# Performance work log

Hardware: AMD Instinct MI355X
Metric: run time of the kernel (lower is better)

## Reference

```python
import jax, jax.numpy as jnp
import numpy as np

_DN = ('NDHWC', 'DHWIO', 'NDHWC')

def _deconv(x, w, b, stride):
    # kernel-3 transposed conv; SAME padding -> out spatial = in * stride
    y = jax.lax.conv_transpose(x, w, strides=(stride, stride, stride),
                               padding='SAME', dimension_numbers=_DN)
    return y + b


def setup_inputs() -> dict:
    key = jax.random.key(0)
    ks = jax.random.split(key, 14)
    C = 128

    def w(k, cin, cout):
        std = 1.0 / np.sqrt(27.0 * cin)  # fan-in init, kernel 3^3
        return jax.random.normal(k, (3, 3, 3, cin, cout), jnp.float32) * std

    def b(k, cout):
        return jax.random.normal(k, (cout,), jnp.float32) * 0.01

    return {
        'x':   jax.random.normal(ks[0], (1, 8, 8, 8, C), jnp.float32),
        'w0':  w(ks[1], C, C),  'b0':  b(ks[2], C),
        'w00': w(ks[3], C, C),  'b00': b(ks[4], C),
        'w1':  w(ks[5], C, C),  'b1':  b(ks[6], C),
        'w10': w(ks[7], C, C),  'b10': b(ks[8], C),
        'w2':  w(ks[9], C, 64), 'b2':  b(ks[10], 64),
        'w20': w(ks[11], 64, 3), 'b20': b(ks[12], 3),
    }


def reference(x, w0, b0, w00, b00, w1, b1, w10, b10, w2, b2, w20, b20):
    # deconv0 (stride 2) -> deconv0_0 (stride 1) -> ReLU
    out = jax.nn.relu(_deconv(_deconv(x, w0, b0, 2), w00, b00, 1))
    # deconv1 (stride 2) -> deconv1_0 (stride 1) -> ReLU
    out = jax.nn.relu(_deconv(_deconv(out, w1, b1, 2), w10, b10, 1))
    # deconv2 (stride 2, C->64) -> deconv2_0 (stride 1, 64->3)
    out = _deconv(_deconv(out, w2, b2, 2), w20, b20, 1)
    return out
```

## Files before the change

kernel.cpp:

```cpp
#include <hip/hip_runtime.h>


typedef __attribute__((ext_vector_type(8))) short bf16x8;
typedef __attribute__((ext_vector_type(8))) _Float16 f16x8;
typedef __attribute__((ext_vector_type(4))) float f32x4;
typedef unsigned short u16;

__device__ __forceinline__ u16 f2bf(float f) {
    unsigned u = __builtin_bit_cast(unsigned, f);
    u += 0x7fffu + ((u >> 16) & 1u);
    return (u16)(u >> 16);
}
__device__ __forceinline__ float bf2f(u16 h) {
    unsigned u = ((unsigned)h) << 16;
    return __builtin_bit_cast(float, u);
}
__device__ __forceinline__ void split_store(float v, u16* ph, u16* pl) {
    u16 h = f2bf(v);
    *ph = h;
    *pl = f2bf(v - bf2f(h));
}
__device__ __forceinline__ u16 f2h(float v) {
    return __builtin_bit_cast(u16, (_Float16)v);
}
__device__ __forceinline__ int swz(int bx, int G) { return (bx & 7) * (G >> 3) + (bx >> 3); }

__global__ __launch_bounds__(256) void pack_all(
    const float* __restrict__ x, float* __restrict__ zf,
    u16* __restrict__ Xh, u16* __restrict__ Xl,
    const float* __restrict__ w0_, const float* __restrict__ w1_,
    const float* __restrict__ w2_, const float* __restrict__ w3_,
    const float* __restrict__ w4_, const float* __restrict__ w5_,
    u16* s0h, u16* s0l, u16* s1h, u16* s1l, u16* s2h, u16* s2l,
    u16* s3h, u16* s3l, u16* s4h, u16* s4l, u16* s5h, u16* s5l)
{
    if (blockIdx.y == 6) {
        if (blockIdx.x < 64) {
            const int i = (blockIdx.x * 256 + threadIdx.x) * 4;
            const float4 v = *(const float4*)(x + i);
            split_store(v.x, Xh + i,     Xl + i);
            split_store(v.y, Xh + i + 1, Xl + i + 1);
            split_store(v.z, Xh + i + 2, Xl + i + 2);
            split_store(v.w, Xh + i + 3, Xl + i + 3);
        } else if (blockIdx.x == 64) {
            ((float4*)zf)[threadIdx.x] = make_float4(0.f, 0.f, 0.f, 0.f);
        }
        return;
    }
    const float* w; u16 *bh, *bl; int Cin, Cout, nNt;
    switch (blockIdx.y) {
        case 0: w = w0_; bh = s0h; bl = s0l; Cin = 128; Cout = 128; nNt = 8; break;
        case 1: w = w1_; bh = s1h; bl = s1l; Cin = 128; Cout = 128; nNt = 8; break;
        case 2: w = w2_; bh = s2h; bl = s2l; Cin = 128; Cout = 128; nNt = 8; break;
        case 3: w = w3_; bh = s3h; bl = s3l; Cin = 128; Cout = 128; nNt = 8; break;
        case 4: w = w4_; bh = s4h; bl = s4l; Cin = 128; Cout = 64;  nNt = 4; break;
        default:w = w5_; bh = s5h; bl = s5l; Cin = 64;  Cout = 3;   nNt = 1; break;
    }
    const bool f16 = (blockIdx.y >= 1);
    const int KC = Cin >> 5;
    const int total = 27 * nNt * KC * 64;
    int t = blockIdx.x * 256 + threadIdx.x;
    if (t >= total) return;
    const int lane = t & 63;
    int r = t >> 6;
    const int kc = r % KC; r /= KC;
    const int nt = r % nNt; r /= nNt;
    const int tap = r;
    const int n  = nt * 16 + (lane & 15);
    const int k0 = kc * 32 + (lane >> 4) * 8;
    const size_t o = (size_t)t * 8;
    for (int j = 0; j < 8; ++j) {
        float v = (n < Cout) ? w[((size_t)tap * Cin + k0 + j) * Cout + n] : 0.f;
        if (f16) {
            const _Float16 h = (_Float16)v;
            bh[o + j] = __builtin_bit_cast(u16, h);
            bl[o + j] = f2h(v - (float)h);
        } else {
            const u16 h = f2bf(v);
            bh[o + j] = h;
            bl[o + j] = f2bf(v - bf2f(h));
        }
    }
}

template<int CIN, int MT, int NT>
__global__ __launch_bounds__(64) void deconv_s2_bf16(
    const u16* __restrict__ Ah, const u16* __restrict__ Al,
    const u16* __restrict__ Bh, const u16* __restrict__ Bl,
    const float* __restrict__ bias, const u16* __restrict__ Z,
    u16* __restrict__ Y, int Din, int lD, int Cout, int nNtTot)
{
    constexpr int KC = CIN >> 5;
    const int Dout = 2 * Din;
    const int lane = threadIdx.x;
    const int ml = lane & 15, kq = lane >> 4;
    const int M0 = swz(blockIdx.x, gridDim.x) * (MT * 16);
    const int N0t = blockIdx.y * NT;
    const int par = blockIdx.z;
    const int rd = (par >> 2) & 1, rh = (par >> 1) & 1, rw = par & 1;

    int sw[MT], sh[MT], sd[MT];
    #pragma unroll
    for (int mt = 0; mt < MT; ++mt) {
        const int sv = M0 + mt * 16 + ml;
        sw[mt] = sv & (Din - 1); sh[mt] = (sv >> lD) & (Din - 1); sd[mt] = sv >> (2 * lD);
    }

    f32x4 acc[MT][NT];
    #pragma unroll
    for (int nt = 0; nt < NT; ++nt) {
        const float bv = bias[(N0t + nt) * 16 + ml];
        #pragma unroll
        for (int mt = 0; mt < MT; ++mt) acc[mt][nt] = (f32x4){bv, bv, bv, bv};
    }

    const int lw = rw ? 0 : 1, lh = rh ? 0 : 1, ld2 = rd ? 0 : 1;
    const int ntap = 1 << (lw + lh + ld2);

    const u16 *pah[MT], *pal[MT];
    size_t fb;
    auto set_tap = [&](int t) {
        const int tw_ = t & ((1 << lw) - 1);
        const int th_ = (t >> lw) & ((1 << lh) - 1);
        const int td_ = t >> (lw + lh);
        const int kd = rd ? 1 : (td_ ? 0 : 2);
        const int kh = rh ? 1 : (th_ ? 0 : 2);
        const int kw = rw ? 1 : (tw_ ? 0 : 2);
        const int dd = rd ? 0 : -td_, dh = rh ? 0 : -th_, dw = rw ? 0 : -tw_;
        const int tap = (kd * 3 + kh) * 3 + kw;
        #pragma unroll
        for (int mt = 0; mt < MT; ++mt) {
            const int id = sd[mt] + dd, ih = sh[mt] + dh, iw = sw[mt] + dw;
            const bool v = id >= 0 && ih >= 0 && iw >= 0;
            const size_t off = (size_t)((id * Din + ih) * Din + iw) * CIN;
            pah[mt] = v ? Ah + off : Z;
            pal[mt] = v ? Al + off : Z;
        }
        fb = ((size_t)tap * nNtTot + N0t) * KC;
    };

    bf16x8 fah[2][MT], fal[2][MT], fbh[2][NT], fbl[2][NT];
    auto load_frags = [&](int buf, int kc) {
        const int ko = kc * 32 + kq * 8;
        #pragma unroll
        for (int mt = 0; mt < MT; ++mt) {
            fah[buf][mt] = *(const bf16x8*)(pah[mt] + ko);
            fal[buf][mt] = *(const bf16x8*)(pal[mt] + ko);
        }
        #pragma unroll
        for (int nt = 0; nt < NT; ++nt) {
            const size_t fo = (fb + (size_t)nt * KC + kc) * 512 + lane * 8;
            fbh[buf][nt] = *(const bf16x8*)(Bh + fo);
            fbl[buf][nt] = *(const bf16x8*)(Bl + fo);
        }
    };

    set_tap(0);
    load_frags(0, 0);

    for (int t = 0; t < ntap; ++t) {
        #pragma unroll
        for (int kc = 0; kc < KC; ++kc) {
            const int cur = kc & 1, nxt = cur ^ 1;
            if (kc + 1 < KC) {
                load_frags(nxt, kc + 1);
            } else {
                set_tap(t + 1 < ntap ? t + 1 : t);
                load_frags(nxt, 0);
            }
            #pragma unroll
            for (int mt = 0; mt < MT; ++mt)
            #pragma unroll
            for (int nt = 0; nt < NT; ++nt) {
                acc[mt][nt] = __builtin_amdgcn_mfma_f32_16x16x32_bf16(fah[cur][mt], fbh[cur][nt], acc[mt][nt], 0, 0, 0);
                acc[mt][nt] = __builtin_amdgcn_mfma_f32_16x16x32_bf16(fah[cur][mt], fbl[cur][nt], acc[mt][nt], 0, 0, 0);
                acc[mt][nt] = __builtin_amdgcn_mfma_f32_16x16x32_bf16(fal[cur][mt], fbh[cur][nt], acc[mt][nt], 0, 0, 0);
            }
        }
    }

    #pragma unroll
    for (int mt = 0; mt < MT; ++mt) {
        #pragma unroll
        for (int r = 0; r < 4; ++r) {
            const int sv = M0 + mt * 16 + kq * 4 + r;
            const int svw = sv & (Din - 1), svh = (sv >> lD) & (Din - 1), svd = sv >> (2 * lD);
            const int od = 2 * svd + rd, oh = 2 * svh + rh, ow = 2 * svw + rw;
            const size_t yb = (size_t)((od * Dout + oh) * Dout + ow) * Cout;
            #pragma unroll
            for (int nt = 0; nt < NT; ++nt)
                Y[yb + (N0t + nt) * 16 + ml] = f2h(acc[mt][nt][r]);
        }
    }
}

template<int CIN, int MT, int NT, bool RELU>
__global__ __launch_bounds__(64) void conv_s1_f16(
    const u16* __restrict__ A, const u16* __restrict__ Bh, const u16* __restrict__ Bl,
    const float* __restrict__ bias, const u16* __restrict__ Z,
    u16* __restrict__ Y, int D, int lD, int Cout, int nNtTot)
{
    constexpr int KC = CIN >> 5;
    const int lane = threadIdx.x;
    const int ml = lane & 15, kq = lane >> 4;
    const int M0 = swz(blockIdx.x, gridDim.x) * (MT * 16);
    const int N0t = blockIdx.y * NT;

    int vw[MT], vh[MT], vd[MT];
    #pragma unroll
    for (int mt = 0; mt < MT; ++mt) {
        const int vox = M0 + mt * 16 + ml;
        vw[mt] = vox & (D - 1); vh[mt] = (vox >> lD) & (D - 1); vd[mt] = vox >> (2 * lD);
    }

    f32x4 acc[MT][NT];
    #pragma unroll
    for (int nt = 0; nt < NT; ++nt) {
        const float bv = bias[(N0t + nt) * 16 + ml];
        #pragma unroll
        for (int mt = 0; mt < MT; ++mt) acc[mt][nt] = (f32x4){bv, bv, bv, bv};
    }

    const u16* pa[MT];
    size_t fb;
    auto set_tap = [&](int tap) {
        const int kd = tap / 9, kh = (tap % 9) / 3, kw = tap % 3;
        #pragma unroll
        for (int mt = 0; mt < MT; ++mt) {
            const int id = vd[mt] + kd - 1, ih = vh[mt] + kh - 1, iw = vw[mt] + kw - 1;
            const bool v = (unsigned)id < (unsigned)D && (unsigned)ih < (unsigned)D &&
                           (unsigned)iw < (unsigned)D;
            pa[mt] = v ? A + (size_t)((id * D + ih) * D + iw) * CIN : Z;
        }
        fb = ((size_t)tap * nNtTot + N0t) * KC;
    };

    f16x8 fa[2][MT], fbh[2][NT], fbl[2][NT];
    auto load_frags = [&](int buf, int kc) {
        const int ko = kc * 32 + kq * 8;
        #pragma unroll
        for (int mt = 0; mt < MT; ++mt)
            fa[buf][mt] = *(const f16x8*)(pa[mt] + ko);
        #pragma unroll
        for (int nt = 0; nt < NT; ++nt) {
            const size_t fo = (fb + (size_t)nt * KC + kc) * 512 + lane * 8;
            fbh[buf][nt] = *(const f16x8*)(Bh + fo);
            fbl[buf][nt] = *(const f16x8*)(Bl + fo);
        }
    };

    set_tap(0);
    load_frags(0, 0);

    for (int tap = 0; tap < 27; ++tap) {
        #pragma unroll
        for (int kc = 0; kc < KC; ++kc) {
            const int cur = kc & 1, nxt = cur ^ 1;
            if (kc + 1 < KC) {
                load_frags(nxt, kc + 1);
            } else {
                set_tap(tap < 26 ? tap + 1 : 26);
                load_frags(nxt, 0);
            }
            #pragma unroll
            for (int mt = 0; mt < MT; ++mt)
            #pragma unroll
            for (int nt = 0; nt < NT; ++nt) {
                acc[mt][nt] = __builtin_amdgcn_mfma_f32_16x16x32_f16(fa[cur][mt], fbh[cur][nt], acc[mt][nt], 0, 0, 0);
                acc[mt][nt] = __builtin_amdgcn_mfma_f32_16x16x32_f16(fa[cur][mt], fbl[cur][nt], acc[mt][nt], 0, 0, 0);
            }
        }
    }

    #pragma unroll
    for (int mt = 0; mt < MT; ++mt) {
        const int vox0 = M0 + mt * 16 + kq * 4;
        #pragma unroll
        for (int nt = 0; nt < NT; ++nt) {
            const int co = (N0t + nt) * 16 + ml;
            #pragma unroll
            for (int r = 0; r < 4; ++r) {
                float v = acc[mt][nt][r];
                if (RELU) v = fmaxf(v, 0.f);
                Y[(size_t)(vox0 + r) * Cout + co] = f2h(v);
            }
        }
    }
}

template<int CIN, int MT, int NT>
__global__ __launch_bounds__(64) void deconv_s2_f16(
    const u16* __restrict__ A, const u16* __restrict__ Bh, const u16* __restrict__ Bl,
    const float* __restrict__ bias, const u16* __restrict__ Z,
    u16* __restrict__ Y, int Din, int lD, int Cout, int nNtTot)
{
    constexpr int KC = CIN >> 5;
    const int Dout = 2 * Din;
    const int lane = threadIdx.x;
    const int ml = lane & 15, kq = lane >> 4;
    const int M0 = swz(blockIdx.x, gridDim.x) * (MT * 16);
    const int N0t = blockIdx.y * NT;
    const int par = blockIdx.z;
    const int rd = (par >> 2) & 1, rh = (par >> 1) & 1, rw = par & 1;

    int sw[MT], sh[MT], sd[MT];
    #pragma unroll
    for (int mt = 0; mt < MT; ++mt) {
        const int sv = M0 + mt * 16 + ml;
        sw[mt] = sv & (Din - 1); sh[mt] = (sv >> lD) & (Din - 1); sd[mt] = sv >> (2 * lD);
    }

    f32x4 acc[MT][NT];
    #pragma unroll
    for (int nt = 0; nt < NT; ++nt) {
        const float bv = bias[(N0t + nt) * 16 + ml];
        #pragma unroll
        for (int mt = 0; mt < MT; ++mt) acc[mt][nt] = (f32x4){bv, bv, bv, bv};
    }

    const int lw = rw ? 0 : 1, lh = rh ? 0 : 1, ld2 = rd ? 0 : 1;
    const int ntap = 1 << (lw + lh + ld2);

    const u16* pa[MT];
    size_t fb;
    auto set_tap = [&](int t) {
        const int tw_ = t & ((1 << lw) - 1);
        const int th_ = (t >> lw) & ((1 << lh) - 1);
        const int td_ = t >> (lw + lh);
        const int kd = rd ? 1 : (td_ ? 0 : 2);
        const int kh = rh ? 1 : (th_ ? 0 : 2);
        const int kw = rw ? 1 : (tw_ ? 0 : 2);
        const int dd = rd ? 0 : -td_, dh = rh ? 0 : -th_, dw = rw ? 0 : -tw_;
        const int tap = (kd * 3 + kh) * 3 + kw;
        #pragma unroll
        for (int mt = 0; mt < MT; ++mt) {
            const int id = sd[mt] + dd, ih = sh[mt] + dh, iw = sw[mt] + dw;
            const bool v = id >= 0 && ih >= 0 && iw >= 0;
            pa[mt] = v ? A + (size_t)((id * Din + ih) * Din + iw) * CIN : Z;
        }
        fb = ((size_t)tap * nNtTot + N0t) * KC;
    };

    f16x8 fa[2][MT], fbh[2][NT], fbl[2][NT];
    auto load_frags = [&](int buf, int kc) {
        const int ko = kc * 32 + kq * 8;
        #pragma unroll
        for (int mt = 0; mt < MT; ++mt)
            fa[buf][mt] = *(const f16x8*)(pa[mt] + ko);
        #pragma unroll
        for (int nt = 0; nt < NT; ++nt) {
            const size_t fo = (fb + (size_t)nt * KC + kc) * 512 + lane * 8;
            fbh[buf][nt] = *(const f16x8*)(Bh + fo);
            fbl[buf][nt] = *(const f16x8*)(Bl + fo);
        }
    };

    set_tap(0);
    load_frags(0, 0);

    for (int t = 0; t < ntap; ++t) {
        #pragma unroll
        for (int kc = 0; kc < KC; ++kc) {
            const int cur = kc & 1, nxt = cur ^ 1;
            if (kc + 1 < KC) {
                load_frags(nxt, kc + 1);
            } else {
                set_tap(t + 1 < ntap ? t + 1 : t);
                load_frags(nxt, 0);
            }
            #pragma unroll
            for (int mt = 0; mt < MT; ++mt)
            #pragma unroll
            for (int nt = 0; nt < NT; ++nt) {
                acc[mt][nt] = __builtin_amdgcn_mfma_f32_16x16x32_f16(fa[cur][mt], fbh[cur][nt], acc[mt][nt], 0, 0, 0);
                acc[mt][nt] = __builtin_amdgcn_mfma_f32_16x16x32_f16(fa[cur][mt], fbl[cur][nt], acc[mt][nt], 0, 0, 0);
            }
        }
    }

    #pragma unroll
    for (int mt = 0; mt < MT; ++mt) {
        #pragma unroll
        for (int r = 0; r < 4; ++r) {
            const int sv = M0 + mt * 16 + kq * 4 + r;
            const int svw = sv & (Din - 1), svh = (sv >> lD) & (Din - 1), svd = sv >> (2 * lD);
            const int od = 2 * svd + rd, oh = 2 * svh + rh, ow = 2 * svw + rw;
            const size_t yb = (size_t)((od * Dout + oh) * Dout + ow) * Cout;
            #pragma unroll
            for (int nt = 0; nt < NT; ++nt)
                Y[yb + (N0t + nt) * 16 + ml] = f2h(acc[mt][nt][r]);
        }
    }
}

template<int D, int R, bool RELU>
__global__ __launch_bounds__(256) void conv_s1_lds_f16(
    const u16* __restrict__ A, const u16* __restrict__ Bh, const u16* __restrict__ Bl,
    const float* __restrict__ bias, u16* __restrict__ Y)
{
    constexpr int SH  = R + 2;
    constexpr int SW  = D + 2;
    constexpr int VST = 72;
    __shared__ u16 sm[3 * SH * SW * VST];

    const int tid  = threadIdx.x;
    const int lane = tid & 63, widx = tid >> 6;
    const int ml = lane & 15, kq = lane >> 4;

    const int bpp = D / R;
    const int lb  = swz(blockIdx.x, gridDim.x);
    const int d   = lb / bpp;
    const int h0  = (lb % bpp) * R;
    const int N0  = widx * 2;

    f32x4 acc[4][2];
    #pragma unroll
    for (int nt = 0; nt < 2; ++nt) {
        const float bv = bias[(N0 + nt) * 16 + ml];
        #pragma unroll
        for (int mt = 0; mt < 4; ++mt) acc[mt][nt] = (f32x4){bv, bv, bv, bv};
    }

    for (int i = tid; i < 3 * SH * 2 * 8; i += 256) {
        const int slot = i >> 3, c8 = i & 7;
        const int side = slot & 1, rr = slot >> 1;
        const int dd = rr / SH, hh = rr % SH;
        *(f16x8*)(sm + ((dd * SH + hh) * SW + (side ? SW - 1 : 0)) * VST + c8 * 8) =
            (f16x8){0,0,0,0,0,0,0,0};
    }

    f16x8 cb[2][2][2], nb[2][2][2];
    auto loadB = [&](f16x8 (&dst)[2][2][2], int kcp, int tap) {
        #pragma unroll
        for (int nt = 0; nt < 2; ++nt)
        #pragma unroll
        for (int kcl = 0; kcl < 2; ++kcl) {
            const size_t fo = (((size_t)tap * 8 + N0 + nt) * 4 + kcp * 2 + kcl) * 512
                            + lane * 8;
            dst[nt][kcl][0] = *(const f16x8*)(Bh + fo);
            dst[nt][kcl][1] = *(const f16x8*)(Bl + fo);
        }
    };
    loadB(cb, 0, 0);

    for (int kcp = 0; kcp < 2; ++kcp) {
        __syncthreads();
        constexpr int NCH = 3 * SH * D * 8;
        for (int i = tid; i < NCH; i += 256) {
            const int vox = i >> 3, c8 = i & 7;
            const int ww = vox % D;
            const int rr = vox / D;
            const int hh = rr % SH, dd = rr / SH;
            const int pd = d + dd - 1, ph = h0 + hh - 1;
            u16* dst = sm + ((dd * SH + hh) * SW + ww + 1) * VST + c8 * 8;
            if ((unsigned)pd < (unsigned)D && (unsigned)ph < (unsigned)D) {
                const size_t g = ((size_t)(pd * D + ph) * D + ww) * 128 + kcp * 64 + c8 * 8;
                *(f16x8*)dst = *(const f16x8*)(A + g);
            } else {
                *(f16x8*)dst = (f16x8){0,0,0,0,0,0,0,0};
            }
        }
        __syncthreads();

        for (int tap = 0; tap < 27; ++tap) {
            const int lin = kcp * 27 + tap + 1;
            if (lin < 54) loadB(nb, lin / 27, lin % 27);
            const int kd = tap / 9, kh = (tap % 9) / 3, kw = tap % 3;
            f16x8 fa[4][2];
            #pragma unroll
            for (int mt = 0; mt < 4; ++mt) {
                const int m = mt * 16 + ml;
                const int mh = m / D, mw = m % D;
                const u16* p = sm + (((kd * SH) + (mh + kh)) * SW + (mw + kw)) * VST;
                fa[mt][0] = *(const f16x8*)(p + kq * 8);
                fa[mt][1] = *(const f16x8*)(p + 32 + kq * 8);
            }
            #pragma unroll
            for (int mt = 0; mt < 4; ++mt)
            #pragma unroll
            for (int nt = 0; nt < 2; ++nt)
            #pragma unroll
            for (int kcl = 0; kcl < 2; ++kcl) {
                acc[mt][nt] = __builtin_amdgcn_mfma_f32_16x16x32_f16(fa[mt][kcl], cb[nt][kcl][0], acc[mt][nt], 0, 0, 0);
                acc[mt][nt] = __builtin_amdgcn_mfma_f32_16x16x32_f16(fa[mt][kcl], cb[nt][kcl][1], acc[mt][nt], 0, 0, 0);
            }
            #pragma unroll
            for (int nt = 0; nt < 2; ++nt)
            #pragma unroll
            for (int kcl = 0; kcl < 2; ++kcl) {
                cb[nt][kcl][0] = nb[nt][kcl][0];
                cb[nt][kcl][1] = nb[nt][kcl][1];
            }
        }
    }

    const size_t M0 = (size_t)(d * D + h0) * D;
    #pragma unroll
    for (int mt = 0; mt < 4; ++mt) {
        #pragma unroll
        for (int nt = 0; nt < 2; ++nt) {
            const int co = (N0 + nt) * 16 + ml;
            #pragma unroll
            for (int r = 0; r < 4; ++r) {
                float v = acc[mt][nt][r];
                if (RELU) v = fmaxf(v, 0.f);
                Y[(M0 + mt * 16 + kq * 4 + r) * 128 + co] = f2h(v);
            }
        }
    }
}

#define L5_VST 72
#define L5_RST (66 * L5_VST)
__global__ __launch_bounds__(256) void conv_c3_lds(
    const u16* __restrict__ A,
    const u16* __restrict__ Bh, const u16* __restrict__ Bl,
    const float* __restrict__ bias, float* __restrict__ out)
{
    __shared__ u16 sm[6 * L5_RST];

    const int tid  = threadIdx.x;
    const int lane = tid & 63, widx = tid >> 6;
    const int ml = lane & 15, kq = lane >> 4;

    const int lb = swz(blockIdx.x, gridDim.x);
    const int d  = lb >> 4;
    const int h0 = (lb & 15) * 4;

    const float bv = (ml < 3) ? bias[ml] : 0.f;
    f32x4 acc[4];
    #pragma unroll
    for (int mt = 0; mt < 4; ++mt) acc[mt] = (f32x4){bv, bv, bv, bv};

    f16x8 cb[2][2], nb[2][2];
    auto loadB = [&](f16x8 (&dst)[2][2], int tap) {
        #pragma unroll
        for (int kcl = 0; kcl < 2; ++kcl) {
            const size_t fo = ((size_t)tap * 2 + kcl) * 512 + lane * 8;
            dst[kcl][0] = *(const f16x8*)(Bh + fo);
            dst[kcl][1] = *(const f16x8*)(Bl + fo);
        }
    };
    loadB(cb, 0);

    for (int kd = 0; kd < 3; ++kd) {
        const int pd = d + kd - 1;
        const bool vpd = (unsigned)pd < 64u;
        __syncthreads();
        #pragma unroll
        for (int i = 0; i < 12; ++i) {
            const int c = tid + 256 * i;
            const int r = c >> 9;
            const int rem = c & 511;
            const int vox = rem >> 3, c8 = rem & 7;
            const int hh = h0 - 1 + r;
            u16* dst = sm + r * L5_RST + (vox + 1) * L5_VST + c8 * 8;
            if (vpd && (unsigned)hh < 64u) {
                const size_t g = (size_t)((pd * 64 + hh) * 64 + vox) * 64 + c8 * 8;
                *(f16x8*)dst = *(const f16x8*)(A + g);
            } else {
                *(f16x8*)dst = (f16x8){0,0,0,0,0,0,0,0};
            }
        }
        if (tid < 96) {
            const int r = tid >> 4, side = (tid >> 3) & 1, c8 = tid & 7;
            *(f16x8*)(sm + r * L5_RST + (side ? 65 : 0) * L5_VST + c8 * 8) =
                (f16x8){0,0,0,0,0,0,0,0};
        }
        __syncthreads();

        #pragma unroll
        for (int t = 0; t < 9; ++t) {
            {
                int lin = kd * 9 + t + 1;
                if (lin > 26) lin = 26;
                loadB(nb, lin);
            }
            const int kh = t / 3, kw = t - kh * 3;
            const int slot = widx + kh;
            #pragma unroll
            for (int mt = 0; mt < 4; ++mt) {
                const u16* p = sm + slot * L5_RST + (mt * 16 + ml + kw) * L5_VST;
                const f16x8 a0 = *(const f16x8*)(p + kq * 8);
                const f16x8 a1 = *(const f16x8*)(p + 32 + kq * 8);
                acc[mt] = __builtin_amdgcn_mfma_f32_16x16x32_f16(a0, cb[0][0], acc[mt], 0, 0, 0);
                acc[mt] = __builtin_amdgcn_mfma_f32_16x16x32_f16(a0, cb[0][1], acc[mt], 0, 0, 0);
                acc[mt] = __builtin_amdgcn_mfma_f32_16x16x32_f16(a1, cb[1][0], acc[mt], 0, 0, 0);
                acc[mt] = __builtin_amdgcn_mfma_f32_16x16x32_f16(a1, cb[1][1], acc[mt], 0, 0, 0);
            }
            #pragma unroll
            for (int kcl = 0; kcl < 2; ++kcl) { cb[kcl][0] = nb[kcl][0]; cb[kcl][1] = nb[kcl][1]; }
        }
    }

    if (ml < 3) {
        const int h = h0 + widx;
        const size_t vb = (size_t)(d * 64 + h) * 64;
        #pragma unroll
        for (int mt = 0; mt < 4; ++mt)
        #pragma unroll
        for (int r = 0; r < 4; ++r)
            out[(vb + mt * 16 + kq * 4 + r) * 3 + ml] = acc[mt][r];
    }
}

extern "C" void kernel_launch(void* const* d_in, const int* in_sizes, int n_in,
                              void* d_out, int out_size, void* d_ws, size_t ws_size,
                              hipStream_t stream)
{
    const float* x   = (const float*)d_in[0];
    const float* w0  = (const float*)d_in[1];  const float* b0  = (const float*)d_in[2];
    const float* w00 = (const float*)d_in[3];  const float* b00 = (const float*)d_in[4];
    const float* w1  = (const float*)d_in[5];  const float* b1  = (const float*)d_in[6];
    const float* w10 = (const float*)d_in[7];  const float* b10 = (const float*)d_in[8];
    const float* w2  = (const float*)d_in[9];  const float* b2  = (const float*)d_in[10];
    const float* w20 = (const float*)d_in[11]; const float* b20 = (const float*)d_in[12];
    float* out = (float*)d_out;

    char* ws = (char*)d_ws;
    float* zf = (float*)ws;
    u16*   Z  = (u16*)ws;
    u16* S4h = (u16*)(ws + 4096);
    u16* S4l = S4h + 221184;
    u16* S5h = S4l + 221184;
    u16* S5l = S5h + 27648;
    u16* Qh  = (u16*)(ws + 1048576);
    u16* Ql  = Qh + 4194304;
    u16* Ph  = (u16*)(ws + 17825792);
    u16* Pl  = Ph + 16777216;
    u16* S1h = (u16*)(ws + 60817408);
    u16* S1l = S1h + 442368;
    u16* S2h = S1l + 442368;
    u16* S2l = S2h + 442368;
    u16* S3h = S2l + 442368;
    u16* S3l = S3h + 442368;
    u16* S0h = S3l + 442368;
    u16* S0l = S0h + 442368;
    u16* Xh  = S0l + 442368;
    u16* Xl  = Xh + 65536;

    pack_all<<<dim3(216, 7), 256, 0, stream>>>(x, zf, Xh, Xl,
        w0, w00, w1, w10, w2, w20,
        S0h, S0l, S1h, S1l, S2h, S2l, S3h, S3l, S4h, S4l, S5h, S5l);

    deconv_s2_bf16<128, 2, 4><<<dim3(16, 2, 8), 64, 0, stream>>>(
        Xh, Xl, S0h, S0l, b0, Z, Ph, 8, 3, 128, 8);

    conv_s1_f16<128, 1, 2, true><<<dim3(256, 4), 64, 0, stream>>>(
        Ph, S1h, S1l, b00, Z, Qh, 16, 4, 128, 8);

    deconv_s2_f16<128, 2, 4><<<dim3(128, 2, 8), 64, 0, stream>>>(
        Qh, S2h, S2l, b1, Z, Ph, 16, 4, 128, 8);

    conv_s1_lds_f16<32, 2, true><<<dim3(512), 256, 0, stream>>>(
        Ph, S3h, S3l, b10, Qh);

    deconv_s2_f16<128, 4, 4><<<dim3(512, 1, 8), 64, 0, stream>>>(
        Qh, S4h, S4l, b2, Z, Ph, 32, 5, 64, 4);

    conv_c3_lds<<<dim3(1024), 256, 0, stream>>>(Ph, S5h, S5l, b20, out);
}
```

Measured before the change: 315.9 us.

## Split channel dimension into two LDS passes in final 64->3 conv

```diff
diff --git a/kernel.cpp b/kernel.cpp
--- a/kernel.cpp
+++ b/kernel.cpp
@@ -510,7 +510,7 @@
     }
 }
 
-#define L5_VST 72
+#define L5_VST 40
 #define L5_RST (66 * L5_VST)
 __global__ __launch_bounds__(256) void conv_c3_lds(
     const u16* __restrict__ A,
@@ -532,64 +532,61 @@
     #pragma unroll
     for (int mt = 0; mt < 4; ++mt) acc[mt] = (f32x4){bv, bv, bv, bv};
 
-    f16x8 cb[2][2], nb[2][2];
-    auto loadB = [&](f16x8 (&dst)[2][2], int tap) {
-        #pragma unroll
-        for (int kcl = 0; kcl < 2; ++kcl) {
-            const size_t fo = ((size_t)tap * 2 + kcl) * 512 + lane * 8;
-            dst[kcl][0] = *(const f16x8*)(Bh + fo);
-            dst[kcl][1] = *(const f16x8*)(Bl + fo);
-        }
-    };
-    loadB(cb, 0);
+    f16x8 cbh, cbl, nbh, nbl;
+    auto loadB = [&](f16x8& dh, f16x8& dl, int tap, int kc) {
+        const size_t fo = ((size_t)tap * 2 + kc) * 512 + lane * 8;
+        dh = *(const f16x8*)(Bh + fo);
+        dl = *(const f16x8*)(Bl + fo);
+    };
+    loadB(cbh, cbl, 0, 0);
 
     for (int kd = 0; kd < 3; ++kd) {
         const int pd = d + kd - 1;
         const bool vpd = (unsigned)pd < 64u;
-        __syncthreads();
-        #pragma unroll
-        for (int i = 0; i < 12; ++i) {
-            const int c = tid + 256 * i;
-            const int r = c >> 9;
-            const int rem = c & 511;
-            const int vox = rem >> 3, c8 = rem & 7;
-            const int hh = h0 - 1 + r;
-            u16* dst = sm + r * L5_RST + (vox + 1) * L5_VST + c8 * 8;
-            if (vpd && (unsigned)hh < 64u) {
-                const size_t g = (size_t)((pd * 64 + hh) * 64 + vox) * 64 + c8 * 8;
-                *(f16x8*)dst = *(const f16x8*)(A + g);
-            } else {
-                *(f16x8*)dst = (f16x8){0,0,0,0,0,0,0,0};
-            }
-        }
-        if (tid < 96) {
-            const int r = tid >> 4, side = (tid >> 3) & 1, c8 = tid & 7;
-            *(f16x8*)(sm + r * L5_RST + (side ? 65 : 0) * L5_VST + c8 * 8) =
-                (f16x8){0,0,0,0,0,0,0,0};
-        }
-        __syncthreads();
-
-        #pragma unroll
-        for (int t = 0; t < 9; ++t) {
-            {
-                int lin = kd * 9 + t + 1;
-                if (lin > 26) lin = 26;
-                loadB(nb, lin);
-            }
-            const int kh = t / 3, kw = t - kh * 3;
-            const int slot = widx + kh;
-            #pragma unroll
-            for (int mt = 0; mt < 4; ++mt) {
-                const u16* p = sm + slot * L5_RST + (mt * 16 + ml + kw) * L5_VST;
-                const f16x8 a0 = *(const f16x8*)(p + kq * 8);
-                const f16x8 a1 = *(const f16x8*)(p + 32 + kq * 8);
-                acc[mt] = __builtin_amdgcn_mfma_f32_16x16x32_f16(a0, cb[0][0], acc[mt], 0, 0, 0);
-                acc[mt] = __builtin_amdgcn_mfma_f32_16x16x32_f16(a0, cb[0][1], acc[mt], 0, 0, 0);
-                acc[mt] = __builtin_amdgcn_mfma_f32_16x16x32_f16(a1, cb[1][0], acc[mt], 0, 0, 0);
-                acc[mt] = __builtin_amdgcn_mfma_f32_16x16x32_f16(a1, cb[1][1], acc[mt], 0, 0, 0);
-            }
-            #pragma unroll
-            for (int kcl = 0; kcl < 2; ++kcl) { cb[kcl][0] = nb[kcl][0]; cb[kcl][1] = nb[kcl][1]; }
+        for (int kc = 0; kc < 2; ++kc) {
+            __syncthreads();
+            #pragma unroll
+            for (int i = 0; i < 6; ++i) {
+                const int c = tid + 256 * i;
+                const int r = c >> 8;
+                const int rem = c & 255;
+                const int vox = rem >> 2, c8 = rem & 3;
+                const int hh = h0 - 1 + r;
+                u16* dst = sm + r * L5_RST + (vox + 1) * L5_VST + c8 * 8;
+                if (vpd && (unsigned)hh < 64u) {
+                    const size_t g = (size_t)((pd * 64 + hh) * 64 + vox) * 64
+                                   + kc * 32 + c8 * 8;
+                    *(f16x8*)dst = *(const f16x8*)(A + g);
+                } else {
+                    *(f16x8*)dst = (f16x8){0,0,0,0,0,0,0,0};
+                }
+            }
+            if (tid < 48) {
+                const int r = tid >> 3, side = (tid >> 2) & 1, c8 = tid & 3;
+                *(f16x8*)(sm + r * L5_RST + (side ? 65 : 0) * L5_VST + c8 * 8) =
+                    (f16x8){0,0,0,0,0,0,0,0};
+            }
+            __syncthreads();
+
+            #pragma unroll
+            for (int t = 0; t < 9; ++t) {
+                {
+                    int lin = (kd * 2 + kc) * 9 + t + 1;
+                    if (lin > 53) lin = 53;
+                    const int Pn = lin / 9, tn = lin - Pn * 9;
+                    loadB(nbh, nbl, (Pn >> 1) * 9 + tn, Pn & 1);
+                }
+                const int kh = t / 3, kw = t - kh * 3;
+                const int slot = widx + kh;
+                #pragma unroll
+                for (int mt = 0; mt < 4; ++mt) {
+                    const u16* p = sm + slot * L5_RST + (mt * 16 + ml + kw) * L5_VST;
+                    const f16x8 af = *(const f16x8*)(p + kq * 8);
+                    acc[mt] = __builtin_amdgcn_mfma_f32_16x16x32_f16(af, cbh, acc[mt], 0, 0, 0);
+                    acc[mt] = __builtin_amdgcn_mfma_f32_16x16x32_f16(af, cbl, acc[mt], 0, 0, 0);
+                }
+                cbh = nbh; cbl = nbl;
+            }
         }
     }
 
```

Measured after the change: 308.7 us. -2.3%, faster.
